# Optimization experiments

Hardware: AMD Instinct MI355X
Metric: run time of the kernel (lower is better)

The kernel has to match this reference:

```python
import jax, jax.numpy as jnp
import numpy as np

T, B, I, H = 2048, 512, 1, 64


def setup_inputs() -> dict:
    key = jax.random.key(0)
    ks = jax.random.split(key, 8)
    s_in = 1.0 / np.sqrt(H)  # torch RNN/Linear init scale (uniform bound)
    return {
        "x": jax.random.normal(ks[0], (T, B, I), dtype=jnp.float32),
        "h": jax.random.normal(ks[1], (1, B, H), dtype=jnp.float32),
        "W_ih": jax.random.uniform(ks[2], (H, I), jnp.float32, -s_in, s_in),
        "W_hh": jax.random.uniform(ks[3], (H, H), jnp.float32, -s_in, s_in),
        "b_ih": jax.random.uniform(ks[4], (H,), jnp.float32, -s_in, s_in),
        "b_hh": jax.random.uniform(ks[5], (H,), jnp.float32, -s_in, s_in),
        "W_lin": jax.random.uniform(ks[6], (1, H), jnp.float32, -s_in, s_in),
        "b_lin": jax.random.uniform(ks[7], (1,), jnp.float32, -s_in, s_in),
    }


def reference(x, h, W_ih, W_hh, b_ih, b_hh, W_lin, b_lin):
    # tanh RNN: h_t = tanh(x_t W_ih^T + b_ih + h_{t-1} W_hh^T + b_hh)
    h0 = h[0]  # [B, H]
    # precompute input projection for all timesteps: [T, B, H]
    xp = jnp.einsum('tbi,hi->tbh', x, W_ih) + b_ih + b_hh

    def step(h_prev, xp_t):
        h_new = jnp.tanh(xp_t + h_prev @ W_hh.T)
        return h_new, h_new

    h_last, hs = jax.lax.scan(step, h0, xp)  # hs: [T, B, H]
    y = jnp.einsum('tbh,oh->tbo', hs, W_lin) + b_lin  # [T, B, 1]
    return y, h_last[None]  # h_n: [1, B, H]
```

## Files before the change

### kernel.cpp

```cpp
#include <hip/hip_runtime.h>

#define TT 2048
#define BB 512
#define HH 64
#define HIST 128
#define HPAD 68

typedef float f32x2 __attribute__((ext_vector_type(2)));
typedef float f32x4 __attribute__((ext_vector_type(4)));

#define FMA2(a, b, c) __builtin_elementwise_fma((a), (b), (c))
#define LO2(q) __builtin_shufflevector((q), (q), 0, 1)
#define HI2(q) __builtin_shufflevector((q), (q), 2, 3)

__global__ __launch_bounds__(64, 1) void rnn_fused(
    const float* __restrict__ x,
    const float* __restrict__ h0,
    const float* __restrict__ Wih,
    const float* __restrict__ Whh,
    const float* __restrict__ bih,
    const float* __restrict__ bhh,
    const float* __restrict__ Wlin,
    const float* __restrict__ blin,
    float* __restrict__ y,
    float* __restrict__ hN)
{
    __shared__ __align__(16) float hist[HIST][HPAD];
    __shared__ float xsh[TT + 4];
    __shared__ __align__(16) float wlin_sh[HH];

    const int b = blockIdx.x;
    const int h = threadIdx.x;

    for (int i = h; i < TT; i += 64)
        xsh[i] = x[(size_t)i * BB + b];
    if (h < 4) xsh[TT + h] = 0.f;

    f32x2 wr[32];
    const float* wp = Whh + h * HH;
#pragma unroll
    for (int i = 0; i < 32; ++i) {
        wr[i][0] = wp[2 * i + 0];
        wr[i][1] = wp[2 * i + 1];
    }
    const float wih  = Wih[h];
    const float bias = bih[h] + bhh[h];
    const float bl   = blin[0];

    wlin_sh[h] = Wlin[h];
    hist[HIST - 1][h] = h0[b * HH + h];

    float hval = 0.f;
    float xw = fmaf(xsh[0], wih, bias);

#pragma unroll 1
    for (int tc = 0; tc < TT; tc += HIST) {
#pragma unroll 4
        for (int ti = 0; ti < HIST; ++ti) {
            const int t  = tc + ti;
            const int rs = (ti + HIST - 1) & (HIST - 1);

            const f32x4* hp = reinterpret_cast<const f32x4*>(&hist[rs][0]);

            f32x2 a01 = {xw, 0.f}, a23 = {0.f, 0.f};
            f32x2 a45 = {0.f, 0.f}, a67 = {0.f, 0.f};
#pragma unroll
            for (int j = 0; j < 4; ++j) {
                const f32x4 p0 = hp[4 * j + 0];
                const f32x4 p1 = hp[4 * j + 1];
                const f32x4 p2 = hp[4 * j + 2];
                const f32x4 p3 = hp[4 * j + 3];
                a01 = FMA2(LO2(p0), wr[8 * j + 0], a01);
                a23 = FMA2(HI2(p0), wr[8 * j + 1], a23);
                a45 = FMA2(LO2(p1), wr[8 * j + 2], a45);
                a67 = FMA2(HI2(p1), wr[8 * j + 3], a67);
                a01 = FMA2(LO2(p2), wr[8 * j + 4], a01);
                a23 = FMA2(HI2(p2), wr[8 * j + 5], a23);
                a45 = FMA2(LO2(p3), wr[8 * j + 6], a45);
                a67 = FMA2(HI2(p3), wr[8 * j + 7], a67);
            }
            const f32x2 s2 = (a01 + a23) + (a45 + a67);
            const float acc = s2[0] + s2[1];

            const float e2 = __builtin_amdgcn_exp2f(acc * 2.885390081777927f);
            const float r  = __builtin_amdgcn_rcpf(e2 + 1.0f);
            hval = fmaf(-2.0f, r, 1.0f);

            hist[ti][h] = hval;

            xw = fmaf(xsh[t + 1], wih, bias);
        }

#pragma unroll 1
        for (int rep = 0; rep < 2; ++rep) {
            const int slot = rep * 64 + h;
            const f32x4* rp = reinterpret_cast<const f32x4*>(&hist[slot][0]);
            const f32x4* wl = reinterpret_cast<const f32x4*>(&wlin_sh[0]);
            f32x2 acc2 = {0.f, 0.f};
#pragma unroll
            for (int i = 0; i < 16; ++i) {
                const f32x4 q  = rp[i];
                const f32x4 qw = wl[i];
                acc2 = FMA2(LO2(q), LO2(qw), acc2);
                acc2 = FMA2(HI2(q), HI2(qw), acc2);
            }
            y[(size_t)(tc + slot) * BB + b] = acc2[0] + acc2[1] + bl;
        }
    }

    hN[b * HH + h] = hval;
}

extern "C" void kernel_launch(void* const* d_in, const int* in_sizes, int n_in,
                              void* d_out, int out_size, void* d_ws, size_t ws_size,
                              hipStream_t stream) {
    const float* x    = (const float*)d_in[0];
    const float* h0   = (const float*)d_in[1];
    const float* Wih  = (const float*)d_in[2];
    const float* Whh  = (const float*)d_in[3];
    const float* bih  = (const float*)d_in[4];
    const float* bhh  = (const float*)d_in[5];
    const float* Wlin = (const float*)d_in[6];
    const float* blin = (const float*)d_in[7];

    float* y  = (float*)d_out;
    float* hN = (float*)d_out + TT * BB;

    rnn_fused<<<dim3(BB), dim3(64), 0, stream>>>(x, h0, Wih, Whh, bih, bhh, Wlin, blin, y, hN);
}
```

Measured before the change: 347.1 us.

## Process two batch rows per wavefront and fold tanh scale into weights

Each 64-thread block now advances two independent batch recurrences, halving the grid to 256 blocks. The recurrent weights held in registers are reused for both rows. The two dependency chains interleave, so LDS and transcendental latency can overlap. The 2/ln2 tanh scale is pre-multiplied into W_hh, W_ih and the bias, which removes a multiply per step, and the history buffer is halved so the output projection runs every 64 steps. The risk is that per-wave serial work doubles, whereas previously two blocks could share a CU on separate SIMDs.

```diff
diff --git a/kernel.cpp b/kernel.cpp
--- a/kernel.cpp
+++ b/kernel.cpp
@@ -3,7 +3,7 @@
 #define TT 2048
 #define BB 512
 #define HH 64
-#define HIST 128
+#define HIST 64
 #define HPAD 68
 
 typedef float f32x2 __attribute__((ext_vector_type(2)));
@@ -25,90 +25,124 @@
     float* __restrict__ y,
     float* __restrict__ hN)
 {
-    __shared__ __align__(16) float hist[HIST][HPAD];
-    __shared__ float xsh[TT + 4];
+    __shared__ __align__(16) float hist[2][HIST][HPAD];
+    __shared__ float xsh[2][TT + 4];
     __shared__ __align__(16) float wlin_sh[HH];
 
-    const int b = blockIdx.x;
-    const int h = threadIdx.x;
+    const int b0 = 2 * blockIdx.x;
+    const int b1 = b0 + 1;
+    const int h  = threadIdx.x;
 
-    for (int i = h; i < TT; i += 64)
-        xsh[i] = x[(size_t)i * BB + b];
-    if (h < 4) xsh[TT + h] = 0.f;
+    for (int i = h; i < TT; i += 64) {
+        xsh[0][i] = x[(size_t)i * BB + b0];
+        xsh[1][i] = x[(size_t)i * BB + b1];
+    }
+    if (h < 4) { xsh[0][TT + h] = 0.f; xsh[1][TT + h] = 0.f; }
+
+    const float KSC = 2.885390081777927f;
 
     f32x2 wr[32];
     const float* wp = Whh + h * HH;
 #pragma unroll
     for (int i = 0; i < 32; ++i) {
-        wr[i][0] = wp[2 * i + 0];
-        wr[i][1] = wp[2 * i + 1];
+        wr[i][0] = wp[2 * i + 0] * KSC;
+        wr[i][1] = wp[2 * i + 1] * KSC;
     }
-    const float wih  = Wih[h];
-    const float bias = bih[h] + bhh[h];
-    const float bl   = blin[0];
+    const float wihs  = Wih[h] * KSC;
+    const float biass = (bih[h] + bhh[h]) * KSC;
+    const float bl    = blin[0];
 
     wlin_sh[h] = Wlin[h];
-    hist[HIST - 1][h] = h0[b * HH + h];
+    hist[0][HIST - 1][h] = h0[b0 * HH + h];
+    hist[1][HIST - 1][h] = h0[b1 * HH + h];
 
-    float hval = 0.f;
-    float xw = fmaf(xsh[0], wih, bias);
+    float hval0 = 0.f, hval1 = 0.f;
+    float xw0 = fmaf(xsh[0][0], wihs, biass);
+    float xw1 = fmaf(xsh[1][0], wihs, biass);
 
 #pragma unroll 1
     for (int tc = 0; tc < TT; tc += HIST) {
-#pragma unroll 4
+#pragma unroll 2
         for (int ti = 0; ti < HIST; ++ti) {
             const int t  = tc + ti;
             const int rs = (ti + HIST - 1) & (HIST - 1);
 
-            const f32x4* hp = reinterpret_cast<const f32x4*>(&hist[rs][0]);
+            const f32x4* hp0 = reinterpret_cast<const f32x4*>(&hist[0][rs][0]);
+            const f32x4* hp1 = reinterpret_cast<const f32x4*>(&hist[1][rs][0]);
 
-            f32x2 a01 = {xw, 0.f}, a23 = {0.f, 0.f};
-            f32x2 a45 = {0.f, 0.f}, a67 = {0.f, 0.f};
+            f32x2 c0a = {xw0, 0.f}, c0b = {0.f, 0.f}, c0c = {0.f, 0.f}, c0d = {0.f, 0.f};
+            f32x2 c1a = {xw1, 0.f}, c1b = {0.f, 0.f}, c1c = {0.f, 0.f}, c1d = {0.f, 0.f};
 #pragma unroll
             for (int j = 0; j < 4; ++j) {
-                const f32x4 p0 = hp[4 * j + 0];
-                const f32x4 p1 = hp[4 * j + 1];
-                const f32x4 p2 = hp[4 * j + 2];
-                const f32x4 p3 = hp[4 * j + 3];
-                a01 = FMA2(LO2(p0), wr[8 * j + 0], a01);
-                a23 = FMA2(HI2(p0), wr[8 * j + 1], a23);
-                a45 = FMA2(LO2(p1), wr[8 * j + 2], a45);
-                a67 = FMA2(HI2(p1), wr[8 * j + 3], a67);
-                a01 = FMA2(LO2(p2), wr[8 * j + 4], a01);
-                a23 = FMA2(HI2(p2), wr[8 * j + 5], a23);
-                a45 = FMA2(LO2(p3), wr[8 * j + 6], a45);
-                a67 = FMA2(HI2(p3), wr[8 * j + 7], a67);
+                const f32x4 p0 = hp0[4 * j + 0];
+                const f32x4 p1 = hp0[4 * j + 1];
+                const f32x4 p2 = hp0[4 * j + 2];
+                const f32x4 p3 = hp0[4 * j + 3];
+                c0a = FMA2(LO2(p0), wr[8 * j + 0], c0a);
+                c0b = FMA2(HI2(p0), wr[8 * j + 1], c0b);
+                c0c = FMA2(LO2(p1), wr[8 * j + 2], c0c);
+                c0d = FMA2(HI2(p1), wr[8 * j + 3], c0d);
+                c0a = FMA2(LO2(p2), wr[8 * j + 4], c0a);
+                c0b = FMA2(HI2(p2), wr[8 * j + 5], c0b);
+                c0c = FMA2(LO2(p3), wr[8 * j + 6], c0c);
+                c0d = FMA2(HI2(p3), wr[8 * j + 7], c0d);
             }
-            const f32x2 s2 = (a01 + a23) + (a45 + a67);
-            const float acc = s2[0] + s2[1];
+#pragma unroll
+            for (int j = 0; j < 4; ++j) {
+                const f32x4 p0 = hp1[4 * j + 0];
+                const f32x4 p1 = hp1[4 * j + 1];
+                const f32x4 p2 = hp1[4 * j + 2];
+                const f32x4 p3 = hp1[4 * j + 3];
+                c1a = FMA2(LO2(p0), wr[8 * j + 0], c1a);
+                c1b = FMA2(HI2(p0), wr[8 * j + 1], c1b);
+                c1c = FMA2(LO2(p1), wr[8 * j + 2], c1c);
+                c1d = FMA2(HI2(p1), wr[8 * j + 3], c1d);
+                c1a = FMA2(LO2(p2), wr[8 * j + 4], c1a);
+                c1b = FMA2(HI2(p2), wr[8 * j + 5], c1b);
+                c1c = FMA2(LO2(p3), wr[8 * j + 6], c1c);
+                c1d = FMA2(HI2(p3), wr[8 * j + 7], c1d);
+            }
+            const f32x2 s20 = (c0a + c0b) + (c0c + c0d);
+            const f32x2 s21 = (c1a + c1b) + (c1c + c1d);
+            const float acc0 = s20[0] + s20[1];
+            const float acc1 = s21[0] + s21[1];
 
-            const float e2 = __builtin_amdgcn_exp2f(acc * 2.885390081777927f);
-            const float r  = __builtin_amdgcn_rcpf(e2 + 1.0f);
-            hval = fmaf(-2.0f, r, 1.0f);
+            const float e20 = __builtin_amdgcn_exp2f(acc0);
+            const float e21 = __builtin_amdgcn_exp2f(acc1);
+            const float r0  = __builtin_amdgcn_rcpf(e20 + 1.0f);
+            const float r1  = __builtin_amdgcn_rcpf(e21 + 1.0f);
+            hval0 = fmaf(-2.0f, r0, 1.0f);
+            hval1 = fmaf(-2.0f, r1, 1.0f);
 
-            hist[ti][h] = hval;
+            hist[0][ti][h] = hval0;
+            hist[1][ti][h] = hval1;
 
-            xw = fmaf(xsh[t + 1], wih, bias);
+            xw0 = fmaf(xsh[0][t + 1], wihs, biass);
+            xw1 = fmaf(xsh[1][t + 1], wihs, biass);
         }
 
-#pragma unroll 1
-        for (int rep = 0; rep < 2; ++rep) {
-            const int slot = rep * 64 + h;
-            const f32x4* rp = reinterpret_cast<const f32x4*>(&hist[slot][0]);
-            const f32x4* wl = reinterpret_cast<const f32x4*>(&wlin_sh[0]);
-            f32x2 acc2 = {0.f, 0.f};
+        {
+            const f32x4* rp0 = reinterpret_cast<const f32x4*>(&hist[0][h][0]);
+            const f32x4* rp1 = reinterpret_cast<const f32x4*>(&hist[1][h][0]);
+            const f32x4* wl  = reinterpret_cast<const f32x4*>(&wlin_sh[0]);
+            f32x2 a0 = {0.f, 0.f}, a1 = {0.f, 0.f};
 #pragma unroll
             for (int i = 0; i < 16; ++i) {
-                const f32x4 q  = rp[i];
                 const f32x4 qw = wl[i];
-                acc2 = FMA2(LO2(q), LO2(qw), acc2);
-                acc2 = FMA2(HI2(q), HI2(qw), acc2);
+                const f32x4 q0 = rp0[i];
+                const f32x4 q1 = rp1[i];
+                a0 = FMA2(LO2(q0), LO2(qw), a0);
+                a0 = FMA2(HI2(q0), HI2(qw), a0);
+                a1 = FMA2(LO2(q1), LO2(qw), a1);
+                a1 = FMA2(HI2(q1), HI2(qw), a1);
             }
-            y[(size_t)(tc + slot) * BB + b] = acc2[0] + acc2[1] + bl;
+            y[(size_t)(tc + h) * BB + b0] = a0[0] + a0[1] + bl;
+            y[(size_t)(tc + h) * BB + b1] = a1[0] + a1[1] + bl;
         }
     }
 
-    hN[b * HH + h] = hval;
+    hN[b0 * HH + h] = hval0;
+    hN[b1 * HH + h] = hval1;
 }
 
 extern "C" void kernel_launch(void* const* d_in, const int* in_sizes, int n_in,
@@ -126,5 +160,5 @@
     float* y  = (float*)d_out;
     float* hN = (float*)d_out + TT * BB;
 
-    rnn_fused<<<dim3(BB), dim3(64), 0, stream>>>(x, h0, Wih, Whh, bih, bhh, Wlin, blin, y, hN);
+    rnn_fused<<<dim3(BB / 2), dim3(64), 0, stream>>>(x, h0, Wih, Whh, bih, bhh, Wlin, blin, y, hN);
 }
```

Result: slower. 899.5 us (+159.2%).

## Replace LDS h-broadcast matvec with DPP/permlane butterfly reduction across lanes

Applied to the files above, without the earlier changes.

The recurrent matvec no longer reads the previous hidden state from shared memory each step. Each lane now keeps its own h value and multiplies it by a permuted column of W_hh. A butterfly of DPP and permlane16/32 swaps then reduces the partial products so that each lane ends up with its own output row. The tanh scale constant is folded into the weights and bias, and the history chunk is shrunk to 64 so the y projection runs with one slot per lane. The aim is to remove the per-step LDS write-then-read dependency and its synchronization latency from the serial chain, at the cost of many cross-lane ops and a correctness risk in the lane mapping.

```diff
diff --git a/kernel.cpp b/kernel.cpp
--- a/kernel.cpp
+++ b/kernel.cpp
@@ -3,15 +3,53 @@
 #define TT 2048
 #define BB 512
 #define HH 64
-#define HIST 128
+#define HIST 64
 #define HPAD 68
 
 typedef float f32x2 __attribute__((ext_vector_type(2)));
 typedef float f32x4 __attribute__((ext_vector_type(4)));
+typedef unsigned uint2v __attribute__((ext_vector_type(2)));
 
 #define FMA2(a, b, c) __builtin_elementwise_fma((a), (b), (c))
 #define LO2(q) __builtin_shufflevector((q), (q), 0, 1)
 #define HI2(q) __builtin_shufflevector((q), (q), 2, 3)
+
+#define DPP_RECV(v, ctrl) \
+    __int_as_float(__builtin_amdgcn_update_dpp(0, __float_as_int(v), (ctrl), 0xF, 0xF, false))
+
+__device__ __forceinline__ int Mmap(int n) {
+    int m = 0;
+    if (n & 1)  m ^= 1;
+    if (n & 2)  m ^= 2;
+    if (n & 4)  m ^= 7;
+    if (n & 8)  m ^= 15;
+    if (n & 16) m ^= 16;
+    if (n & 32) m ^= 32;
+    return m;
+}
+
+__device__ __forceinline__ float recv16(float v) {
+#if __has_builtin(__builtin_amdgcn_permlane16_swap)
+    uint2v r = __builtin_amdgcn_permlane16_swap(__float_as_uint(v), __float_as_uint(v), false, false);
+    return (__uint_as_float(r[0]) + __uint_as_float(r[1])) - v;
+#else
+    float a = v, b = v;
+    asm volatile("s_nop 1\n\tv_permlane16_swap_b32 %0, %1" : "+v"(a), "+v"(b));
+    return (a + b) - v;
+#endif
+}
+__device__ __forceinline__ float recv32(float v) {
+#if __has_builtin(__builtin_amdgcn_permlane32_swap)
+    uint2v r = __builtin_amdgcn_permlane32_swap(__float_as_uint(v), __float_as_uint(v), false, false);
+    return (__uint_as_float(r[0]) + __uint_as_float(r[1])) - v;
+#else
+    float a = v, b = v;
+    asm volatile("s_nop 1\n\tv_permlane32_swap_b32 %0, %1" : "+v"(a), "+v"(b));
+    return (a + b) - v;
+#endif
+}
+
+#define Q(n) qv[(n) >> 1][(n) & 1]
 
 __global__ __launch_bounds__(64, 1) void rnn_fused(
     const float* __restrict__ x,
@@ -25,90 +63,88 @@
     float* __restrict__ y,
     float* __restrict__ hN)
 {
+    __shared__ float wsh[HH * HH];
+    __shared__ float xsh[TT + 4];
     __shared__ __align__(16) float hist[HIST][HPAD];
-    __shared__ float xsh[TT + 4];
     __shared__ __align__(16) float wlin_sh[HH];
 
     const int b = blockIdx.x;
     const int h = threadIdx.x;
 
-    for (int i = h; i < TT; i += 64)
-        xsh[i] = x[(size_t)i * BB + b];
+    for (int i = h; i < HH * HH; i += 64) wsh[i] = Whh[i];
+    for (int i = h; i < TT; i += 64)      xsh[i] = x[(size_t)i * BB + b];
     if (h < 4) xsh[TT + h] = 0.f;
+    wlin_sh[h] = Wlin[h];
 
-    f32x2 wr[32];
-    const float* wp = Whh + h * HH;
+    const float KSC = 2.885390081777927f;
+
+    f32x2 wc[32];
 #pragma unroll
-    for (int i = 0; i < 32; ++i) {
-        wr[i][0] = wp[2 * i + 0];
-        wr[i][1] = wp[2 * i + 1];
+    for (int n = 0; n < 64; n += 2) {
+        wc[n >> 1][0] = wsh[((h ^ Mmap(n))     << 6) | h] * KSC;
+        wc[n >> 1][1] = wsh[((h ^ Mmap(n + 1)) << 6) | h] * KSC;
     }
-    const float wih  = Wih[h];
-    const float bias = bih[h] + bhh[h];
-    const float bl   = blin[0];
+    const float wihs  = Wih[h] * KSC;
+    const float biass = (bih[h] + bhh[h]) * KSC;
+    const float bl    = blin[0];
 
-    wlin_sh[h] = Wlin[h];
-    hist[HIST - 1][h] = h0[b * HH + h];
-
-    float hval = 0.f;
-    float xw = fmaf(xsh[0], wih, bias);
+    float hval = h0[(size_t)b * HH + h];
+    float xw   = fmaf(xsh[0], wihs, biass);
 
 #pragma unroll 1
     for (int tc = 0; tc < TT; tc += HIST) {
-#pragma unroll 4
+#pragma unroll 2
         for (int ti = 0; ti < HIST; ++ti) {
-            const int t  = tc + ti;
-            const int rs = (ti + HIST - 1) & (HIST - 1);
+            const int t = tc + ti;
 
-            const f32x4* hp = reinterpret_cast<const f32x4*>(&hist[rs][0]);
+            const f32x2 hv2 = {hval, hval};
+            f32x2 qv[32];
+            {
+                const f32x2 seed = {xw, 0.f};
+                qv[0] = FMA2(wc[0], hv2, seed);
+            }
+#pragma unroll
+            for (int i = 1; i < 32; ++i) qv[i] = wc[i] * hv2;
 
-            f32x2 a01 = {xw, 0.f}, a23 = {0.f, 0.f};
-            f32x2 a45 = {0.f, 0.f}, a67 = {0.f, 0.f};
 #pragma unroll
-            for (int j = 0; j < 4; ++j) {
-                const f32x4 p0 = hp[4 * j + 0];
-                const f32x4 p1 = hp[4 * j + 1];
-                const f32x4 p2 = hp[4 * j + 2];
-                const f32x4 p3 = hp[4 * j + 3];
-                a01 = FMA2(LO2(p0), wr[8 * j + 0], a01);
-                a23 = FMA2(HI2(p0), wr[8 * j + 1], a23);
-                a45 = FMA2(LO2(p1), wr[8 * j + 2], a45);
-                a67 = FMA2(HI2(p1), wr[8 * j + 3], a67);
-                a01 = FMA2(LO2(p2), wr[8 * j + 4], a01);
-                a23 = FMA2(HI2(p2), wr[8 * j + 5], a23);
-                a45 = FMA2(LO2(p3), wr[8 * j + 6], a45);
-                a67 = FMA2(HI2(p3), wr[8 * j + 7], a67);
-            }
-            const f32x2 s2 = (a01 + a23) + (a45 + a67);
-            const float acc = s2[0] + s2[1];
+            for (int n = 0; n < 64; n += 2)  Q(n) += DPP_RECV(Q(n + 1), 0xB1);
+#pragma unroll
+            for (int n = 0; n < 64; n += 4)  Q(n) += DPP_RECV(Q(n + 2), 0x4E);
+#pragma unroll
+            for (int n = 0; n < 64; n += 8)  Q(n) += DPP_RECV(Q(n + 4), 0x141);
+#pragma unroll
+            for (int n = 0; n < 64; n += 16) Q(n) += DPP_RECV(Q(n + 8), 0x140);
+            Q(0)  += recv16(Q(16));
+            Q(32) += recv16(Q(48));
+            Q(0)  += recv32(Q(32));
 
-            const float e2 = __builtin_amdgcn_exp2f(acc * 2.885390081777927f);
+            const float acc = Q(0);
+
+            const float e2 = __builtin_amdgcn_exp2f(acc);
             const float r  = __builtin_amdgcn_rcpf(e2 + 1.0f);
             hval = fmaf(-2.0f, r, 1.0f);
 
             hist[ti][h] = hval;
 
-            xw = fmaf(xsh[t + 1], wih, bias);
+            xw = fmaf(xsh[t + 1], wihs, biass);
         }
 
-#pragma unroll 1
-        for (int rep = 0; rep < 2; ++rep) {
-            const int slot = rep * 64 + h;
-            const f32x4* rp = reinterpret_cast<const f32x4*>(&hist[slot][0]);
+        {
+            const f32x4* rp = reinterpret_cast<const f32x4*>(&hist[h][0]);
             const f32x4* wl = reinterpret_cast<const f32x4*>(&wlin_sh[0]);
-            f32x2 acc2 = {0.f, 0.f};
+            f32x2 a2 = {0.f, 0.f};
 #pragma unroll
             for (int i = 0; i < 16; ++i) {
-                const f32x4 q  = rp[i];
+                const f32x4 qq = rp[i];
                 const f32x4 qw = wl[i];
-                acc2 = FMA2(LO2(q), LO2(qw), acc2);
-                acc2 = FMA2(HI2(q), HI2(qw), acc2);
+                a2 = FMA2(LO2(qq), LO2(qw), a2);
+                a2 = FMA2(HI2(qq), HI2(qw), a2);
             }
-            y[(size_t)(tc + slot) * BB + b] = acc2[0] + acc2[1] + bl;
+            y[(size_t)(tc + h) * BB + b] = a2[0] + a2[1] + bl;
         }
     }
 
-    hN[b * HH + h] = hval;
+    hN[(size_t)b * HH + h] = hval;
 }
 
 extern "C" void kernel_launch(void* const* d_in, const int* in_sizes, int n_in,
```

Result: slower. 625.7 us (+80.3%).

## Split hidden-state matvec K across lane quads with DPP reduction

Applied to the files above, without the earlier changes.

Each lane now handles four output neurons over a 16-wide slice of the hidden state instead of one neuron over all 64. Partial sums are combined across the four lanes with DPP adds. This cuts per-step LDS reads from 64 floats to 16 per lane, targeting the LDS bandwidth and latency on the serial recurrence. The tanh scale constant is folded into the weights and bias, and the history buffer is halved to 64 steps so the output projection runs once per chunk. The cost is extra cross-lane reduction and select operations on the critical path.

```diff
diff --git a/kernel.cpp b/kernel.cpp
--- a/kernel.cpp
+++ b/kernel.cpp
@@ -3,7 +3,7 @@
 #define TT 2048
 #define BB 512
 #define HH 64
-#define HIST 128
+#define HIST 64
 #define HPAD 68
 
 typedef float f32x2 __attribute__((ext_vector_type(2)));
@@ -12,6 +12,9 @@
 #define FMA2(a, b, c) __builtin_elementwise_fma((a), (b), (c))
 #define LO2(q) __builtin_shufflevector((q), (q), 0, 1)
 #define HI2(q) __builtin_shufflevector((q), (q), 2, 3)
+
+#define DPP_ADD(v, ctrl) \
+    ((v) + __int_as_float(__builtin_amdgcn_update_dpp(0, __float_as_int(v), (ctrl), 0xF, 0xF, false)))
 
 __global__ __launch_bounds__(64, 1) void rnn_fused(
     const float* __restrict__ x,
@@ -25,90 +28,118 @@
     float* __restrict__ y,
     float* __restrict__ hN)
 {
+    __shared__ float wsh[HH * HH];
+    __shared__ float xsh[TT + 4];
     __shared__ __align__(16) float hist[HIST][HPAD];
-    __shared__ float xsh[TT + 4];
     __shared__ __align__(16) float wlin_sh[HH];
 
-    const int b = blockIdx.x;
-    const int h = threadIdx.x;
+    const int b    = blockIdx.x;
+    const int lane = threadIdx.x;
+    const int hl   = lane >> 2;
+    const int ks   = lane & 3;
+    const int d    = ks * 16 + hl;
 
-    for (int i = h; i < TT; i += 64)
-        xsh[i] = x[(size_t)i * BB + b];
-    if (h < 4) xsh[TT + h] = 0.f;
+    for (int i = lane; i < HH * HH; i += 64) wsh[i] = Whh[i];
+    for (int i = lane; i < TT; i += 64)      xsh[i] = x[(size_t)i * BB + b];
+    if (lane < 4) xsh[TT + lane] = 0.f;
+    wlin_sh[lane] = Wlin[lane];
+
+    const float KSC = 2.885390081777927f;
 
     f32x2 wr[32];
-    const float* wp = Whh + h * HH;
 #pragma unroll
-    for (int i = 0; i < 32; ++i) {
-        wr[i][0] = wp[2 * i + 0];
-        wr[i][1] = wp[2 * i + 1];
+    for (int g = 0; g < 4; ++g) {
+        const float* row = &wsh[(g * 16 + hl) * HH + ks * 16];
+#pragma unroll
+        for (int i = 0; i < 8; ++i) {
+            wr[g * 8 + i][0] = row[2 * i + 0] * KSC;
+            wr[g * 8 + i][1] = row[2 * i + 1] * KSC;
+        }
     }
-    const float wih  = Wih[h];
-    const float bias = bih[h] + bhh[h];
-    const float bl   = blin[0];
+    const float wihs  = Wih[d] * KSC;
+    const float biass = (bih[d] + bhh[d]) * KSC;
+    const float bl    = blin[0];
 
-    wlin_sh[h] = Wlin[h];
-    hist[HIST - 1][h] = h0[b * HH + h];
-
+    hist[HIST - 1][d] = h0[(size_t)b * HH + d];
     float hval = 0.f;
-    float xw = fmaf(xsh[0], wih, bias);
+    float xw   = fmaf(xsh[0], wihs, biass);
 
 #pragma unroll 1
     for (int tc = 0; tc < TT; tc += HIST) {
-#pragma unroll 4
+#pragma unroll 2
         for (int ti = 0; ti < HIST; ++ti) {
             const int t  = tc + ti;
             const int rs = (ti + HIST - 1) & (HIST - 1);
 
-            const f32x4* hp = reinterpret_cast<const f32x4*>(&hist[rs][0]);
+            const f32x4* hp = reinterpret_cast<const f32x4*>(&hist[rs][ks * 16]);
+            const f32x4 p0 = hp[0], p1 = hp[1], p2 = hp[2], p3 = hp[3];
+            const f32x2 d0 = LO2(p0), d1 = HI2(p0), d2 = LO2(p1), d3 = HI2(p1);
+            const f32x2 d4 = LO2(p2), d5 = HI2(p2), d6 = LO2(p3), d7 = HI2(p3);
 
-            f32x2 a01 = {xw, 0.f}, a23 = {0.f, 0.f};
-            f32x2 a45 = {0.f, 0.f}, a67 = {0.f, 0.f};
-#pragma unroll
-            for (int j = 0; j < 4; ++j) {
-                const f32x4 p0 = hp[4 * j + 0];
-                const f32x4 p1 = hp[4 * j + 1];
-                const f32x4 p2 = hp[4 * j + 2];
-                const f32x4 p3 = hp[4 * j + 3];
-                a01 = FMA2(LO2(p0), wr[8 * j + 0], a01);
-                a23 = FMA2(HI2(p0), wr[8 * j + 1], a23);
-                a45 = FMA2(LO2(p1), wr[8 * j + 2], a45);
-                a67 = FMA2(HI2(p1), wr[8 * j + 3], a67);
-                a01 = FMA2(LO2(p2), wr[8 * j + 4], a01);
-                a23 = FMA2(HI2(p2), wr[8 * j + 5], a23);
-                a45 = FMA2(LO2(p3), wr[8 * j + 6], a45);
-                a67 = FMA2(HI2(p3), wr[8 * j + 7], a67);
-            }
-            const f32x2 s2 = (a01 + a23) + (a45 + a67);
-            const float acc = s2[0] + s2[1];
+            f32x2 g0a = {0.f, 0.f}, g0b = {0.f, 0.f};
+            f32x2 g1a = {0.f, 0.f}, g1b = {0.f, 0.f};
+            f32x2 g2a = {0.f, 0.f}, g2b = {0.f, 0.f};
+            f32x2 g3a = {0.f, 0.f}, g3b = {0.f, 0.f};
+            g0a = FMA2(d0, wr[0],  g0a); g0b = FMA2(d1, wr[1],  g0b);
+            g0a = FMA2(d2, wr[2],  g0a); g0b = FMA2(d3, wr[3],  g0b);
+            g0a = FMA2(d4, wr[4],  g0a); g0b = FMA2(d5, wr[5],  g0b);
+            g0a = FMA2(d6, wr[6],  g0a); g0b = FMA2(d7, wr[7],  g0b);
+            g1a = FMA2(d0, wr[8],  g1a); g1b = FMA2(d1, wr[9],  g1b);
+            g1a = FMA2(d2, wr[10], g1a); g1b = FMA2(d3, wr[11], g1b);
+            g1a = FMA2(d4, wr[12], g1a); g1b = FMA2(d5, wr[13], g1b);
+            g1a = FMA2(d6, wr[14], g1a); g1b = FMA2(d7, wr[15], g1b);
+            g2a = FMA2(d0, wr[16], g2a); g2b = FMA2(d1, wr[17], g2b);
+            g2a = FMA2(d2, wr[18], g2a); g2b = FMA2(d3, wr[19], g2b);
+            g2a = FMA2(d4, wr[20], g2a); g2b = FMA2(d5, wr[21], g2b);
+            g2a = FMA2(d6, wr[22], g2a); g2b = FMA2(d7, wr[23], g2b);
+            g3a = FMA2(d0, wr[24], g3a); g3b = FMA2(d1, wr[25], g3b);
+            g3a = FMA2(d2, wr[26], g3a); g3b = FMA2(d3, wr[27], g3b);
+            g3a = FMA2(d4, wr[28], g3a); g3b = FMA2(d5, wr[29], g3b);
+            g3a = FMA2(d6, wr[30], g3a); g3b = FMA2(d7, wr[31], g3b);
 
-            const float e2 = __builtin_amdgcn_exp2f(acc * 2.885390081777927f);
+            const f32x2 h0v = g0a + g0b, h1v = g1a + g1b;
+            const f32x2 h2v = g2a + g2b, h3v = g3a + g3b;
+            float s0 = h0v[0] + h0v[1];
+            float s1 = h1v[0] + h1v[1];
+            float s2 = h2v[0] + h2v[1];
+            float s3 = h3v[0] + h3v[1];
+
+            s0 = DPP_ADD(s0, 0xB1); s0 = DPP_ADD(s0, 0x4E);
+            s1 = DPP_ADD(s1, 0xB1); s1 = DPP_ADD(s1, 0x4E);
+            s2 = DPP_ADD(s2, 0xB1); s2 = DPP_ADD(s2, 0x4E);
+            s3 = DPP_ADD(s3, 0xB1); s3 = DPP_ADD(s3, 0x4E);
+
+            const float sA = (ks & 1) ? s1 : s0;
+            const float sB = (ks & 1) ? s3 : s2;
+            const float s  = (ks & 2) ? sB : sA;
+
+            const float acc = s + xw;
+
+            const float e2 = __builtin_amdgcn_exp2f(acc);
             const float r  = __builtin_amdgcn_rcpf(e2 + 1.0f);
             hval = fmaf(-2.0f, r, 1.0f);
 
-            hist[ti][h] = hval;
+            hist[ti][d] = hval;
 
-            xw = fmaf(xsh[t + 1], wih, bias);
+            xw = fmaf(xsh[t + 1], wihs, biass);
         }
 
-#pragma unroll 1
-        for (int rep = 0; rep < 2; ++rep) {
-            const int slot = rep * 64 + h;
-            const f32x4* rp = reinterpret_cast<const f32x4*>(&hist[slot][0]);
+        {
+            const f32x4* rp = reinterpret_cast<const f32x4*>(&hist[lane][0]);
             const f32x4* wl = reinterpret_cast<const f32x4*>(&wlin_sh[0]);
-            f32x2 acc2 = {0.f, 0.f};
+            f32x2 a2 = {0.f, 0.f};
 #pragma unroll
             for (int i = 0; i < 16; ++i) {
-                const f32x4 q  = rp[i];
+                const f32x4 qq = rp[i];
                 const f32x4 qw = wl[i];
-                acc2 = FMA2(LO2(q), LO2(qw), acc2);
-                acc2 = FMA2(HI2(q), HI2(qw), acc2);
+                a2 = FMA2(LO2(qq), LO2(qw), a2);
+                a2 = FMA2(HI2(qq), HI2(qw), a2);
             }
-            y[(size_t)(tc + slot) * BB + b] = acc2[0] + acc2[1] + bl;
+            y[(size_t)(tc + lane) * BB + b] = a2[0] + a2[1] + bl;
         }
     }
 
-    hN[b * HH + h] = hval;
+    hN[(size_t)b * HH + d] = hval;
 }
 
 extern "C" void kernel_launch(void* const* d_in, const int* in_sizes, int n_in,
```

New measurement: 381.4 us. 9.9% more time.
